# Kernel optimization log

Measured on AMD Instinct MI355X. Metric: run time of the kernel, lower is better.

## Reference

```python
import jax, jax.numpy as jnp
import numpy as np

BIT = 64
NUM_TRAIN = 200000
BATCH = 256
NUM_CLASSES = 100
MAX_SAMPLE = 30          # max_SampleNum in original
ALPHA = 0.01             # config['alpha']
M = 2 * BIT              # self.m = 2 * bit


def setup_inputs() -> dict:
    key = jax.random.key(0)
    k1, k2, k3, k4, k5 = jax.random.split(key, 5)
    u = jax.random.normal(k1, (BATCH, BIT), dtype=jnp.float32)
    y = jax.random.randint(k2, (BATCH,), 0, NUM_CLASSES)
    # distinct scatter targets into the bank, like dataloader sample indices
    ind = jax.random.choice(k3, NUM_TRAIN, (BATCH,), replace=False)
    U = jax.random.normal(k4, (NUM_TRAIN, BIT), dtype=jnp.float32)
    Y = jax.random.randint(k5, (NUM_TRAIN,), 0, NUM_CLASSES).astype(jnp.float32)
    return {"u": u, "y": y, "ind": ind, "U": U, "Y": Y}


def reference(u, y, ind, U, Y):
    yf = y.astype(jnp.float32)
    # scatter update of the memory bank (u.data -> detached in original)
    U = U.at[ind].set(jax.lax.stop_gradient(u))
    Y = Y.at[ind].set(yf)

    # For each sample, the first MAX_SAMPLE ascending indices with Y == y[i]
    # (same as torch.where(self.Y == indx)[0][:max_SampleNum]).
    match = (Y[None, :] == yf[:, None])                       # (B, N)
    pos = jnp.arange(NUM_TRAIN, dtype=jnp.int32)
    # matched positions keep their index; unmatched get index + N -> sorted after
    key_mat = jnp.where(match, pos[None, :], pos[None, :] + NUM_TRAIN)  # (B, N)
    _, order = jax.lax.top_k(-key_mat, MAX_SAMPLE)            # (B, 30) ascending matched idx first
    count = jnp.minimum(match.sum(axis=1), MAX_SAMPLE)        # per-row pool size
    valid = (jnp.arange(MAX_SAMPLE)[None, :] < count[:, None]).reshape(-1)  # (B*30,)

    pool_idx = order.reshape(-1)                              # (P,) P = B*30
    U_pool = U[pool_idx]                                      # (P, bit)
    Y_pool = Y[pool_idx]                                      # (P,)

    # pairwise squared distance u vs pool
    dist = jnp.sum((u[:, None, :] - U_pool[None, :, :]) ** 2, axis=2)  # (B, P)
    mism = (yf[:, None] != Y_pool[None, :]).astype(jnp.float32)        # (B, P)
    pair = (1.0 - mism) * 0.5 * dist + mism * 0.5 * jnp.clip(M - dist, 0.0)

    vmask = valid.astype(jnp.float32)[None, :]
    step = jnp.sum(valid.astype(jnp.float32))                 # dynamic pool length in original
    loss1 = jnp.sum(pair * vmask) / (u.shape[0] * step)       # == loss.mean() over (B, step)
    loss2 = ALPHA * jnp.mean(jnp.abs(jnp.abs(u) - 1.0))
    return loss1 + loss2
```

## Files before the change

kernel.cpp:

```cpp
#include <hip/hip_runtime.h>

#define NTRAIN 200000
#define NB     256
#define BIT    64
#define MAXS   30
#define NCLS   100
#define ESPL   8
#define EPB    4
#define CHUNK  4096
#define PERT   16
#define NREG   16
#define MVAL   128.0f
#define ALPHA  0.01f

__global__ __launch_bounds__(256) void dsh_main_kernel(
    const float* __restrict__ u, const int* __restrict__ y,
    const int* __restrict__ ind, const float* __restrict__ U,
    const float* __restrict__ Y,
    float* __restrict__ partial, int* __restrict__ cntw)
{
    __shared__ int   ovrT[CHUNK];
    __shared__ float up_l[EPB * BIT];
    __shared__ int   ind_l[NB];
    __shared__ int   y_l[NB];
    __shared__ int   pool[MAXS];
    __shared__ int   povr[EPB];
    __shared__ int   wsum[4];
    __shared__ float red[4];

    const int t    = threadIdx.x;
    const int j    = blockIdx.x;
    const int lane = t & 63;
    const int wave = t >> 6;

    if (j >= NCLS * ESPL) {
        const int q = j - NCLS * ESPL;
        float4 v = ((const float4*)u)[q * 256 + t];
        float a = fabsf(fabsf(v.x) - 1.f) + fabsf(fabsf(v.y) - 1.f)
                + fabsf(fabsf(v.z) - 1.f) + fabsf(fabsf(v.w) - 1.f);
        #pragma unroll
        for (int off = 32; off; off >>= 1) a += __shfl_down(a, off, 64);
        if (lane == 0) red[wave] = a;
        __syncthreads();
        if (t == 0) partial[j] = red[0] + red[1] + red[2] + red[3];
        return;
    }

    const int c = j >> 3;
    const int e = j & 7;

    ind_l[t] = ind[t];
    y_l[t]   = y[t];
    __syncthreads();

    unsigned long long bal = __ballot(y_l[t] == c);
    if (lane == 0) wsum[wave] = (int)__popcll(bal);
    __syncthreads();
    const int mult = wsum[0] + wsum[1] + wsum[2] + wsum[3];
    if (mult == 0) {
        if (t == 0) { partial[j] = 0.f; if (e == 0) cntw[c] = 0; }
        return;
    }
    __syncthreads();

    const float cf = (float)c;

    int count = 0;
    for (int base = 0; base < NTRAIN && count < MAXS; base += CHUNK) {
        const int s = base + t * PERT;
        float yf[PERT];
        if (s < NTRAIN) {
            #pragma unroll
            for (int q2 = 0; q2 < 4; ++q2)
                ((float4*)yf)[q2] = ((const float4*)(Y + s))[q2];
        }
        #pragma unroll
        for (int k2 = 0; k2 < 4; ++k2)
            ((int4*)ovrT)[t + 256 * k2] = make_int4(-1, -1, -1, -1);
        __syncthreads();
        unsigned rel = (unsigned)(ind_l[t] - base);
        if (rel < (unsigned)CHUNK)
            ovrT[(rel & 15) * 256 + (rel >> 4)] = t;
        __syncthreads();

        unsigned mbits = 0; int mcnt = 0;
        if (s < NTRAIN) {
            #pragma unroll
            for (int k2 = 0; k2 < PERT; ++k2) {
                int o = ovrT[k2 * 256 + t];
                bool m = (o >= 0) ? (y_l[o] == c) : (yf[k2] == cf);
                if (m) { mbits |= (1u << k2); ++mcnt; }
            }
        }
        int x = mcnt;
        #pragma unroll
        for (int off = 1; off < 64; off <<= 1) {
            int v = __shfl_up(x, off, 64);
            if (lane >= off) x += v;
        }
        if (lane == 63) wsum[wave] = x;
        __syncthreads();
        int wpre = 0;
        #pragma unroll
        for (int w = 0; w < 4; ++w) if (w < wave) wpre += wsum[w];
        int r = count + wpre + (x - mcnt);
        #pragma unroll
        for (int k2 = 0; k2 < PERT; ++k2) {
            if ((mbits >> k2) & 1u) {
                if (r < MAXS) pool[r] = s + k2;
                ++r;
            }
        }
        count += wsum[0] + wsum[1] + wsum[2] + wsum[3];
        __syncthreads();
    }
    const int cnt = (count < MAXS) ? count : MAXS;

    const int p0 = e * EPB;
    const int pe = (p0 + EPB < cnt) ? p0 + EPB : cnt;
    if (t < EPB) povr[t] = -1;
    __syncthreads();
    for (int k2 = p0; k2 < pe; ++k2)
        if (ind_l[t] == pool[k2]) povr[k2 - p0] = t;
    __syncthreads();
    {
        const int pp = t >> 6;
        const int d  = t & 63;
        float v = 0.f;
        if (p0 + pp < pe) {
            const int ov = povr[pp];
            v = (ov >= 0) ? u[ov * BIT + d] : U[pool[p0 + pp] * BIT + d];
        }
        up_l[t] = v;
    }
    __syncthreads();

    float4 ur[16];
    {
        const float4* urp = (const float4*)(u + t * BIT);
        #pragma unroll
        for (int q2 = 0; q2 < 16; ++q2) ur[q2] = urp[q2];
    }
    const bool same = (y_l[t] == c);
    const int npool = pe - p0;
    float acc = 0.f;
    for (int pp = 0; pp < npool; ++pp) {
        const float4* up = (const float4*)(up_l + pp * BIT);
        float d0 = 0.f, d1 = 0.f, d2 = 0.f, d3 = 0.f;
        #pragma unroll
        for (int q2 = 0; q2 < 16; ++q2) {
            float4 v = up[q2];
            float a0 = ur[q2].x - v.x; d0 += a0 * a0;
            float a1 = ur[q2].y - v.y; d1 += a1 * a1;
            float a2 = ur[q2].z - v.z; d2 += a2 * a2;
            float a3 = ur[q2].w - v.w; d3 += a3 * a3;
        }
        const float dist = (d0 + d1) + (d2 + d3);
        acc += same ? dist : fmaxf(MVAL - dist, 0.f);
    }

    #pragma unroll
    for (int off = 32; off; off >>= 1) acc += __shfl_down(acc, off, 64);
    if (lane == 0) red[wave] = acc;
    __syncthreads();
    if (t == 0) {
        partial[j] = (float)mult * (red[0] + red[1] + red[2] + red[3]);
        if (e == 0) cntw[c] = mult * cnt;
    }
}

__global__ __launch_bounds__(256) void dsh_final_kernel(
    const float* __restrict__ partial, const int* __restrict__ cntw,
    float* __restrict__ out)
{
    const int t = threadIdx.x;
    const int lane = t & 63, wave = t >> 6;
    __shared__ float redp[4], reda[4];
    __shared__ int   redc[4];

    float p = 0.f, a = 0.f;
    #pragma unroll
    for (int k = 0; k < 4; ++k) {
        const int idx = t + 256 * k;
        if (idx < NCLS * ESPL)            p += partial[idx];
        else if (idx < NCLS * ESPL + NREG) a += partial[idx];
    }
    int cc = (t < NCLS) ? cntw[t] : 0;
    #pragma unroll
    for (int off = 32; off; off >>= 1) {
        p  += __shfl_down(p,  off, 64);
        a  += __shfl_down(a,  off, 64);
        cc += __shfl_down(cc, off, 64);
    }
    if (lane == 0) { redp[wave] = p; reda[wave] = a; redc[wave] = cc; }
    __syncthreads();
    if (t == 0) {
        float P = redp[0] + redp[1] + redp[2] + redp[3];
        float A = reda[0] + reda[1] + reda[2] + reda[3];
        int   S = redc[0] + redc[1] + redc[2] + redc[3];
        out[0] = 0.5f * P / (256.0f * (float)S) + ALPHA * (A * (1.0f / 16384.0f));
    }
}

extern "C" void kernel_launch(void* const* d_in, const int* in_sizes, int n_in,
                              void* d_out, int out_size, void* d_ws, size_t ws_size,
                              hipStream_t stream) {
    const float* u   = (const float*)d_in[0];
    const int*   y   = (const int*)d_in[1];
    const int*   ind = (const int*)d_in[2];
    const float* U   = (const float*)d_in[3];
    const float* Y   = (const float*)d_in[4];
    float* out = (float*)d_out;

    float* partial = (float*)d_ws;
    int*   cntw    = (int*)((char*)d_ws + 4096);

    dsh_main_kernel<<<dim3(NCLS * ESPL + NREG), dim3(256), 0, stream>>>(
        u, y, ind, U, Y, partial, cntw);
    dsh_final_kernel<<<dim3(1), dim3(256), 0, stream>>>(partial, cntw, out);
}
```

Baseline: 22.17 us.

## Fuse final reduction via last-block atomic and replace LDS override table with sparse fix-lists

Merges the final reduction into the main kernel: each block bumps an atomic counter and the last block to finish does the final sum, which removes the second kernel launch. That launch is replaced by a memset of the counter. The per-chunk 4096-entry LDS override table is also replaced by small lists of bank positions whose label changes to or from class c after the scatter update, and each thread patches its match bits from those lists. This cuts shared-memory traffic and barriers in the scan loop and adds launch_bounds occupancy hints, at the cost of an extra memset and the atomic fence.

```diff
diff --git a/kernel.cpp b/kernel.cpp
--- a/kernel.cpp
+++ b/kernel.cpp
@@ -10,180 +10,204 @@
 #define CHUNK  4096
 #define PERT   16
 #define NREG   16
+#define NCLSB  (NCLS * ESPL)
+#define GRID_N (NCLSB + NREG)
 #define MVAL   128.0f
 #define ALPHA  0.01f
 
-__global__ __launch_bounds__(256) void dsh_main_kernel(
+__global__ __launch_bounds__(256, 4) void dsh_fused_kernel(
     const float* __restrict__ u, const int* __restrict__ y,
     const int* __restrict__ ind, const float* __restrict__ U,
     const float* __restrict__ Y,
-    float* __restrict__ partial, int* __restrict__ cntw)
+    float* __restrict__ partial, int* __restrict__ cntw,
+    int* __restrict__ counter, float* __restrict__ out)
 {
-    __shared__ int   ovrT[CHUNK];
+    __shared__ int   y_l[NB];
+    __shared__ int   ind_l[NB];
+    __shared__ int   addl[NB];
+    __shared__ int   reml[NB];
     __shared__ float up_l[EPB * BIT];
-    __shared__ int   ind_l[NB];
-    __shared__ int   y_l[NB];
     __shared__ int   pool[MAXS];
     __shared__ int   povr[EPB];
-    __shared__ int   wsum[4];
-    __shared__ float red[4];
+    __shared__ int   wsA[4], wsB[4], wsC[4];
+    __shared__ float redf[4], redg[4];
+    __shared__ int   redi[4];
+    __shared__ int   lastflag;
 
     const int t    = threadIdx.x;
     const int j    = blockIdx.x;
     const int lane = t & 63;
     const int wave = t >> 6;
 
-    if (j >= NCLS * ESPL) {
-        const int q = j - NCLS * ESPL;
+    float myPartial = 0.f;
+    int   myCntW    = -1;
+
+    if (j >= NCLSB) {
+        const int q = j - NCLSB;
         float4 v = ((const float4*)u)[q * 256 + t];
         float a = fabsf(fabsf(v.x) - 1.f) + fabsf(fabsf(v.y) - 1.f)
                 + fabsf(fabsf(v.z) - 1.f) + fabsf(fabsf(v.w) - 1.f);
         #pragma unroll
         for (int off = 32; off; off >>= 1) a += __shfl_down(a, off, 64);
-        if (lane == 0) red[wave] = a;
+        if (lane == 0) redf[wave] = a;
         __syncthreads();
-        if (t == 0) partial[j] = red[0] + red[1] + red[2] + red[3];
-        return;
-    }
-
-    const int c = j >> 3;
-    const int e = j & 7;
-
-    ind_l[t] = ind[t];
-    y_l[t]   = y[t];
+        myPartial = redf[0] + redf[1] + redf[2] + redf[3];
+    } else {
+        const int c = j >> 3;
+        const int e = j & 7;
+        const float cf = (float)c;
+
+        const int myi = ind[t];
+        const int myy = y[t];
+        ind_l[t] = myi;
+        y_l[t]   = myy;
+        const float ybank = Y[myi];
+
+        const bool ismem = (myy == c);
+        const bool fneg  = ismem && (ybank != cf);
+        const bool fpos  = (!ismem) && (ybank == cf);
+        unsigned long long balm = __ballot(ismem);
+        unsigned long long bala = __ballot(fneg);
+        unsigned long long balr = __ballot(fpos);
+        if (lane == 0) {
+            wsA[wave] = (int)__popcll(balm);
+            wsB[wave] = (int)__popcll(bala);
+            wsC[wave] = (int)__popcll(balr);
+        }
+        __syncthreads();
+        const int mult = wsA[0] + wsA[1] + wsA[2] + wsA[3];
+        const int nadd = wsB[0] + wsB[1] + wsB[2] + wsB[3];
+        const int nrem = wsC[0] + wsC[1] + wsC[2] + wsC[3];
+
+        if (mult > 0) {
+            int pa = 0, pr = 0;
+            #pragma unroll
+            for (int w = 0; w < 4; ++w) if (w < wave) { pa += wsB[w]; pr += wsC[w]; }
+            const unsigned long long lm = (1ull << lane) - 1ull;
+            if (fneg) addl[pa + (int)__popcll(bala & lm)] = myi;
+            if (fpos) reml[pr + (int)__popcll(balr & lm)] = myi;
+            __syncthreads();
+
+            int count = 0;
+            for (int base = 0; base < NTRAIN && count < MAXS; base += CHUNK) {
+                const int s = base + t * PERT;
+                unsigned mbits = 0;
+                int mcnt = 0;
+                if (s < NTRAIN) {
+                    const float4* yp = (const float4*)(Y + s);
+                    #pragma unroll
+                    for (int q2 = 0; q2 < 4; ++q2) {
+                        float4 v = yp[q2];
+                        if (v.x == cf) mbits |= 1u << (q2 * 4 + 0);
+                        if (v.y == cf) mbits |= 1u << (q2 * 4 + 1);
+                        if (v.z == cf) mbits |= 1u << (q2 * 4 + 2);
+                        if (v.w == cf) mbits |= 1u << (q2 * 4 + 3);
+                    }
+                    for (int a2 = 0; a2 < nadd; ++a2) {
+                        unsigned rel = (unsigned)(addl[a2] - s);
+                        if (rel < (unsigned)PERT) mbits |= 1u << rel;
+                    }
+                    for (int r2 = 0; r2 < nrem; ++r2) {
+                        unsigned rel = (unsigned)(reml[r2] - s);
+                        if (rel < (unsigned)PERT) mbits &= ~(1u << rel);
+                    }
+                    mcnt = __popc(mbits);
+                }
+                int x = mcnt;
+                #pragma unroll
+                for (int off = 1; off < 64; off <<= 1) {
+                    int v2 = __shfl_up(x, off, 64);
+                    if (lane >= off) x += v2;
+                }
+                if (lane == 63) wsA[wave] = x;
+                __syncthreads();
+                int r = count + (x - mcnt);
+                #pragma unroll
+                for (int w = 0; w < 4; ++w) if (w < wave) r += wsA[w];
+                #pragma unroll
+                for (int k = 0; k < PERT; ++k) {
+                    if ((mbits >> k) & 1u) {
+                        if (r < MAXS) pool[r] = s + k;
+                        ++r;
+                    }
+                }
+                count += wsA[0] + wsA[1] + wsA[2] + wsA[3];
+                __syncthreads();
+            }
+            const int cnt = (count < MAXS) ? count : MAXS;
+
+            float4 ur[16];
+            {
+                const float4* urp = (const float4*)(u + t * BIT);
+                #pragma unroll
+                for (int q2 = 0; q2 < 16; ++q2) ur[q2] = urp[q2];
+            }
+
+            const int p0 = e * EPB;
+            const int pe = (p0 + EPB < cnt) ? p0 + EPB : cnt;
+            if (t < EPB) povr[t] = -1;
+            __syncthreads();
+            for (int k2 = p0; k2 < pe; ++k2)
+                if (myi == pool[k2]) povr[k2 - p0] = t;
+            __syncthreads();
+            {
+                const int pp = t >> 6;
+                const int d  = t & 63;
+                float v = 0.f;
+                if (p0 + pp < pe) {
+                    const int ov = povr[pp];
+                    v = (ov >= 0) ? u[ov * BIT + d] : U[pool[p0 + pp] * BIT + d];
+                }
+                up_l[t] = v;
+            }
+            __syncthreads();
+
+            const bool same = (myy == c);
+            const int npool = pe - p0;
+            float acc = 0.f;
+            for (int pp = 0; pp < npool; ++pp) {
+                const float4* up = (const float4*)(up_l + pp * BIT);
+                float d0 = 0.f, d1 = 0.f, d2 = 0.f, d3 = 0.f;
+                #pragma unroll
+                for (int q2 = 0; q2 < 16; ++q2) {
+                    float4 v = up[q2];
+                    float a0 = ur[q2].x - v.x; d0 += a0 * a0;
+                    float a1 = ur[q2].y - v.y; d1 += a1 * a1;
+                    float a2 = ur[q2].z - v.z; d2 += a2 * a2;
+                    float a3 = ur[q2].w - v.w; d3 += a3 * a3;
+                }
+                const float dist = (d0 + d1) + (d2 + d3);
+                acc += same ? dist : fmaxf(MVAL - dist, 0.f);
+            }
+            #pragma unroll
+            for (int off = 32; off; off >>= 1) acc += __shfl_down(acc, off, 64);
+            if (lane == 0) redf[wave] = acc;
+            __syncthreads();
+            myPartial = (float)mult * (redf[0] + redf[1] + redf[2] + redf[3]);
+            if (e == 0) myCntW = mult * cnt;
+        } else {
+            myPartial = 0.f;
+            if (e == 0) myCntW = 0;
+        }
+    }
+
+    if (t == 0) {
+        partial[j] = myPartial;
+        if (myCntW >= 0) cntw[j >> 3] = myCntW;
+        __threadfence();
+        int old = __hip_atomic_fetch_add(counter, 1, __ATOMIC_ACQ_REL,
+                                         __HIP_MEMORY_SCOPE_AGENT);
+        lastflag = (old == GRID_N - 1);
+    }
     __syncthreads();
-
-    unsigned long long bal = __ballot(y_l[t] == c);
-    if (lane == 0) wsum[wave] = (int)__popcll(bal);
-    __syncthreads();
-    const int mult = wsum[0] + wsum[1] + wsum[2] + wsum[3];
-    if (mult == 0) {
-        if (t == 0) { partial[j] = 0.f; if (e == 0) cntw[c] = 0; }
-        return;
-    }
-    __syncthreads();
-
-    const float cf = (float)c;
-
-    int count = 0;
-    for (int base = 0; base < NTRAIN && count < MAXS; base += CHUNK) {
-        const int s = base + t * PERT;
-        float yf[PERT];
-        if (s < NTRAIN) {
-            #pragma unroll
-            for (int q2 = 0; q2 < 4; ++q2)
-                ((float4*)yf)[q2] = ((const float4*)(Y + s))[q2];
-        }
-        #pragma unroll
-        for (int k2 = 0; k2 < 4; ++k2)
-            ((int4*)ovrT)[t + 256 * k2] = make_int4(-1, -1, -1, -1);
-        __syncthreads();
-        unsigned rel = (unsigned)(ind_l[t] - base);
-        if (rel < (unsigned)CHUNK)
-            ovrT[(rel & 15) * 256 + (rel >> 4)] = t;
-        __syncthreads();
-
-        unsigned mbits = 0; int mcnt = 0;
-        if (s < NTRAIN) {
-            #pragma unroll
-            for (int k2 = 0; k2 < PERT; ++k2) {
-                int o = ovrT[k2 * 256 + t];
-                bool m = (o >= 0) ? (y_l[o] == c) : (yf[k2] == cf);
-                if (m) { mbits |= (1u << k2); ++mcnt; }
-            }
-        }
-        int x = mcnt;
-        #pragma unroll
-        for (int off = 1; off < 64; off <<= 1) {
-            int v = __shfl_up(x, off, 64);
-            if (lane >= off) x += v;
-        }
-        if (lane == 63) wsum[wave] = x;
-        __syncthreads();
-        int wpre = 0;
-        #pragma unroll
-        for (int w = 0; w < 4; ++w) if (w < wave) wpre += wsum[w];
-        int r = count + wpre + (x - mcnt);
-        #pragma unroll
-        for (int k2 = 0; k2 < PERT; ++k2) {
-            if ((mbits >> k2) & 1u) {
-                if (r < MAXS) pool[r] = s + k2;
-                ++r;
-            }
-        }
-        count += wsum[0] + wsum[1] + wsum[2] + wsum[3];
-        __syncthreads();
-    }
-    const int cnt = (count < MAXS) ? count : MAXS;
-
-    const int p0 = e * EPB;
-    const int pe = (p0 + EPB < cnt) ? p0 + EPB : cnt;
-    if (t < EPB) povr[t] = -1;
-    __syncthreads();
-    for (int k2 = p0; k2 < pe; ++k2)
-        if (ind_l[t] == pool[k2]) povr[k2 - p0] = t;
-    __syncthreads();
-    {
-        const int pp = t >> 6;
-        const int d  = t & 63;
-        float v = 0.f;
-        if (p0 + pp < pe) {
-            const int ov = povr[pp];
-            v = (ov >= 0) ? u[ov * BIT + d] : U[pool[p0 + pp] * BIT + d];
-        }
-        up_l[t] = v;
-    }
-    __syncthreads();
-
-    float4 ur[16];
-    {
-        const float4* urp = (const float4*)(u + t * BIT);
-        #pragma unroll
-        for (int q2 = 0; q2 < 16; ++q2) ur[q2] = urp[q2];
-    }
-    const bool same = (y_l[t] == c);
-    const int npool = pe - p0;
-    float acc = 0.f;
-    for (int pp = 0; pp < npool; ++pp) {
-        const float4* up = (const float4*)(up_l + pp * BIT);
-        float d0 = 0.f, d1 = 0.f, d2 = 0.f, d3 = 0.f;
-        #pragma unroll
-        for (int q2 = 0; q2 < 16; ++q2) {
-            float4 v = up[q2];
-            float a0 = ur[q2].x - v.x; d0 += a0 * a0;
-            float a1 = ur[q2].y - v.y; d1 += a1 * a1;
-            float a2 = ur[q2].z - v.z; d2 += a2 * a2;
-            float a3 = ur[q2].w - v.w; d3 += a3 * a3;
-        }
-        const float dist = (d0 + d1) + (d2 + d3);
-        acc += same ? dist : fmaxf(MVAL - dist, 0.f);
-    }
-
-    #pragma unroll
-    for (int off = 32; off; off >>= 1) acc += __shfl_down(acc, off, 64);
-    if (lane == 0) red[wave] = acc;
-    __syncthreads();
-    if (t == 0) {
-        partial[j] = (float)mult * (red[0] + red[1] + red[2] + red[3]);
-        if (e == 0) cntw[c] = mult * cnt;
-    }
-}
-
-__global__ __launch_bounds__(256) void dsh_final_kernel(
-    const float* __restrict__ partial, const int* __restrict__ cntw,
-    float* __restrict__ out)
-{
-    const int t = threadIdx.x;
-    const int lane = t & 63, wave = t >> 6;
-    __shared__ float redp[4], reda[4];
-    __shared__ int   redc[4];
+    if (!lastflag) return;
 
     float p = 0.f, a = 0.f;
     #pragma unroll
     for (int k = 0; k < 4; ++k) {
         const int idx = t + 256 * k;
-        if (idx < NCLS * ESPL)            p += partial[idx];
-        else if (idx < NCLS * ESPL + NREG) a += partial[idx];
+        if (idx < NCLSB)       p += partial[idx];
+        else if (idx < GRID_N) a += partial[idx];
     }
     int cc = (t < NCLS) ? cntw[t] : 0;
     #pragma unroll
@@ -192,12 +216,12 @@
         a  += __shfl_down(a,  off, 64);
         cc += __shfl_down(cc, off, 64);
     }
-    if (lane == 0) { redp[wave] = p; reda[wave] = a; redc[wave] = cc; }
+    if (lane == 0) { redf[wave] = p; redg[wave] = a; redi[wave] = cc; }
     __syncthreads();
     if (t == 0) {
-        float P = redp[0] + redp[1] + redp[2] + redp[3];
-        float A = reda[0] + reda[1] + reda[2] + reda[3];
-        int   S = redc[0] + redc[1] + redc[2] + redc[3];
+        const float P = redf[0] + redf[1] + redf[2] + redf[3];
+        const float A = redg[0] + redg[1] + redg[2] + redg[3];
+        const int   S = redi[0] + redi[1] + redi[2] + redi[3];
         out[0] = 0.5f * P / (256.0f * (float)S) + ALPHA * (A * (1.0f / 16384.0f));
     }
 }
@@ -214,8 +238,9 @@
 
     float* partial = (float*)d_ws;
     int*   cntw    = (int*)((char*)d_ws + 4096);
-
-    dsh_main_kernel<<<dim3(NCLS * ESPL + NREG), dim3(256), 0, stream>>>(
-        u, y, ind, U, Y, partial, cntw);
-    dsh_final_kernel<<<dim3(1), dim3(256), 0, stream>>>(partial, cntw, out);
+    int*   counter = (int*)((char*)d_ws + 8192);
+
+    hipMemsetAsync(counter, 0, sizeof(int), stream);
+    dsh_fused_kernel<<<dim3(GRID_N), dim3(256), 0, stream>>>(
+        u, y, ind, U, Y, partial, cntw, counter, out);
 }
```

Measured after the change: 44.87 us. 102% more time.
